# Performance work log

Measured on AMD Instinct MI355X. Metric: run time of the kernel, lower is better.

Reference implementation:

```python
import jax, jax.numpy as jnp
import numpy as np

STATE_DIM = 64
MEASURE_DIM = 32
N = 1048576  # measurement batch (broadcast column dim of z)


def setup_inputs() -> dict:
    key = jax.random.key(0)
    kz, kf = jax.random.split(key)
    z = jax.random.normal(kz, (MEASURE_DIM, N), dtype=jnp.float32)
    # Parameters initialized as in AKF.__init__ (identity matrices), with a
    # small perturbation on F so the dynamics are non-trivial but S stays
    # well-conditioned for the inverse.
    F = jnp.eye(STATE_DIM, dtype=jnp.float32) + 0.01 * jax.random.normal(kf, (STATE_DIM, STATE_DIM), dtype=jnp.float32)
    H = jnp.eye(MEASURE_DIM, STATE_DIM, dtype=jnp.float32)
    Q = jnp.eye(STATE_DIM, dtype=jnp.float32)
    R = jnp.eye(MEASURE_DIM, dtype=jnp.float32)
    P = jnp.eye(STATE_DIM, dtype=jnp.float32)
    x = jnp.zeros((STATE_DIM, 1), dtype=jnp.float32)
    return {"z": z, "F": F, "H": H, "Q": Q, "R": R, "P": P, "x": x}


def reference(z, F, H, Q, R, P, x):
    # One Kalman filter update step (predict + correct), batched over N
    # measurement columns in z. Returns the updated state estimate, matching
    # the torch module's `return self.x`.
    x_pred = F @ x                      # [s, 1]
    P_pred = F @ P @ F.T + Q            # [s, s]
    y = z - H @ x_pred                  # [m, N] (broadcast of [m,1])
    S = H @ P_pred @ H.T + R            # [m, m]
    K = P_pred @ H.T @ jnp.linalg.inv(S)  # [s, m]
    x_new = x_pred + K @ y              # [s, N]
    return x_new
```

## Files before the change

### kernel.cpp

```cpp
#include <hip/hip_runtime.h>

#define SD 64
#define MD 32

__global__ __launch_bounds__(256) void akf_prepare(
    const float* __restrict__ F, const float* __restrict__ H,
    const float* __restrict__ Q, const float* __restrict__ R,
    const float* __restrict__ P, const float* __restrict__ x,
    float* __restrict__ Kb)
{
    __shared__ float sT[SD * SD];
    __shared__ float sPp[SD * SD];
    __shared__ float sHP[MD * SD];
    __shared__ float sAug[MD][2 * MD];
    __shared__ float sK[SD * MD];
    __shared__ float sxp[SD];
    __shared__ float sHx[MD];
    __shared__ float sfac[MD];
    __shared__ float spiv;

    const int tid = threadIdx.x;

    if (tid < SD) {
        float a = 0.f;
        for (int k = 0; k < SD; ++k) a += F[tid * SD + k] * x[k];
        sxp[tid] = a;
    }
    for (int idx = tid; idx < SD * SD; idx += 256) {
        int i = idx >> 6, j = idx & 63;
        float a = 0.f;
        for (int k = 0; k < SD; ++k) a += F[i * SD + k] * P[k * SD + j];
        sT[idx] = a;
    }
    __syncthreads();

    for (int idx = tid; idx < SD * SD; idx += 256) {
        int i = idx >> 6, j = idx & 63;
        float a = Q[idx];
        for (int k = 0; k < SD; ++k) a += sT[i * SD + k] * F[j * SD + k];
        sPp[idx] = a;
    }
    __syncthreads();

    for (int idx = tid; idx < MD * SD; idx += 256) {
        int i = idx >> 6, j = idx & 63;
        float a = 0.f;
        for (int k = 0; k < SD; ++k) a += H[i * SD + k] * sPp[k * SD + j];
        sHP[idx] = a;
    }
    if (tid < MD) {
        float a = 0.f;
        for (int k = 0; k < SD; ++k) a += H[tid * SD + k] * sxp[k];
        sHx[tid] = a;
    }
    __syncthreads();

    for (int idx = tid; idx < MD * MD; idx += 256) {
        int i = idx >> 5, j = idx & 31;
        float a = R[idx];
        for (int k = 0; k < SD; ++k) a += sHP[i * SD + k] * H[j * SD + k];
        sAug[i][j] = a;
        sAug[i][MD + j] = (i == j) ? 1.f : 0.f;
    }
    __syncthreads();

    for (int kp = 0; kp < MD; ++kp) {
        if (tid == 0) spiv = 1.f / sAug[kp][kp];
        __syncthreads();
        if (tid < 2 * MD) sAug[kp][tid] *= spiv;
        __syncthreads();
        if (tid < MD) sfac[tid] = (tid == kp) ? 0.f : sAug[tid][kp];
        __syncthreads();
        for (int idx = tid; idx < MD * 2 * MD; idx += 256) {
            int i = idx >> 6, j = idx & 63;
            if (i != kp) sAug[i][j] -= sfac[i] * sAug[kp][j];
        }
        __syncthreads();
    }

    for (int idx = tid; idx < SD * MD; idx += 256) {
        int i = idx >> 5, j = idx & 31;
        float a = 0.f;
        for (int k = 0; k < SD; ++k) a += sPp[i * SD + k] * H[j * SD + k];
        sT[idx] = a;
    }
    __syncthreads();

    for (int idx = tid; idx < SD * MD; idx += 256) {
        int i = idx >> 5, j = idx & 31;
        float a = 0.f;
        for (int k = 0; k < MD; ++k) a += sT[i * MD + k] * sAug[k][MD + j];
        sK[idx] = a;
        Kb[idx] = a;
    }
    __syncthreads();

    if (tid < SD) {
        float a = sxp[tid];
        for (int j = 0; j < MD; ++j) a -= sK[tid * MD + j] * sHx[j];
        Kb[SD * MD + tid] = a;
    }
}

__global__ __launch_bounds__(256) void akf_apply(
    const float* __restrict__ z, const float* __restrict__ Kb,
    float* __restrict__ out, int N)
{
    __shared__ float sK[SD * MD];
    __shared__ float sb[SD];

    const int tid = threadIdx.x;
    for (int idx = tid; idx < SD * MD; idx += 256) sK[idx] = Kb[idx];
    if (tid < SD) sb[tid] = Kb[SD * MD + tid];
    __syncthreads();

    const int c = (blockIdx.x * 256 + tid) * 4;
    if (c >= N) return;

    float4 zv[MD];
#pragma unroll
    for (int j = 0; j < MD; ++j)
        zv[j] = *(const float4*)(z + (size_t)j * N + c);

#pragma unroll 2
    for (int i = 0; i < SD; ++i) {
        const float bi = sb[i];
        float4 acc = make_float4(bi, bi, bi, bi);
#pragma unroll
        for (int j = 0; j < MD; j += 4) {
            const float4 k4 = *(const float4*)(&sK[i * MD + j]);
            acc.x = fmaf(k4.x, zv[j].x, acc.x);
            acc.y = fmaf(k4.x, zv[j].y, acc.y);
            acc.z = fmaf(k4.x, zv[j].z, acc.z);
            acc.w = fmaf(k4.x, zv[j].w, acc.w);
            acc.x = fmaf(k4.y, zv[j + 1].x, acc.x);
            acc.y = fmaf(k4.y, zv[j + 1].y, acc.y);
            acc.z = fmaf(k4.y, zv[j + 1].z, acc.z);
            acc.w = fmaf(k4.y, zv[j + 1].w, acc.w);
            acc.x = fmaf(k4.z, zv[j + 2].x, acc.x);
            acc.y = fmaf(k4.z, zv[j + 2].y, acc.y);
            acc.z = fmaf(k4.z, zv[j + 2].z, acc.z);
            acc.w = fmaf(k4.z, zv[j + 2].w, acc.w);
            acc.x = fmaf(k4.w, zv[j + 3].x, acc.x);
            acc.y = fmaf(k4.w, zv[j + 3].y, acc.y);
            acc.z = fmaf(k4.w, zv[j + 3].z, acc.z);
            acc.w = fmaf(k4.w, zv[j + 3].w, acc.w);
        }
        *(float4*)(out + (size_t)i * N + c) = acc;
    }
}

extern "C" void kernel_launch(void* const* d_in, const int* in_sizes, int n_in,
                              void* d_out, int out_size, void* d_ws, size_t ws_size,
                              hipStream_t stream)
{
    const float* z = (const float*)d_in[0];
    const float* F = (const float*)d_in[1];
    const float* H = (const float*)d_in[2];
    const float* Q = (const float*)d_in[3];
    const float* R = (const float*)d_in[4];
    const float* P = (const float*)d_in[5];
    const float* x = (const float*)d_in[6];
    float* out = (float*)d_out;
    float* Kb = (float*)d_ws;

    const int N = in_sizes[0] / MD;

    akf_prepare<<<1, 256, 0, stream>>>(F, H, Q, R, P, x, Kb);

    const int cols_per_block = 256 * 4;
    const int nblocks = (N + cols_per_block - 1) / cols_per_block;
    akf_apply<<<nblocks, 256, 0, stream>>>(z, Kb, out, N);
}
```

Baseline: 469.4 us.

## Rewrite prepare kernel with 1024 threads and shuffle-based inverse; stream apply kernel

```diff
diff --git a/kernel.cpp b/kernel.cpp
--- a/kernel.cpp
+++ b/kernel.cpp
@@ -3,101 +3,154 @@
 #define SD 64
 #define MD 32
 
-__global__ __launch_bounds__(256) void akf_prepare(
+typedef float f32x4 __attribute__((ext_vector_type(4)));
+
+__global__ __launch_bounds__(1024) void akf_prepare(
     const float* __restrict__ F, const float* __restrict__ H,
     const float* __restrict__ Q, const float* __restrict__ R,
     const float* __restrict__ P, const float* __restrict__ x,
     float* __restrict__ Kb)
 {
-    __shared__ float sT[SD * SD];
-    __shared__ float sPp[SD * SD];
-    __shared__ float sHP[MD * SD];
-    __shared__ float sAug[MD][2 * MD];
-    __shared__ float sK[SD * MD];
-    __shared__ float sxp[SD];
-    __shared__ float sHx[MD];
-    __shared__ float sfac[MD];
-    __shared__ float spiv;
+    __shared__ __align__(16) float sF [SD * SD];
+    __shared__ __align__(16) float sFt[SD * 68];
+    __shared__ __align__(16) float sP [SD * SD];
+    __shared__ __align__(16) float sT [SD * 68];
+    __shared__ __align__(16) float sPp[SD * 68];
+    __shared__ __align__(16) float sH [MD * SD];
+    __shared__ __align__(16) float sHt[SD * 36];
+    __shared__ __align__(16) float sA [SD * 36];
+    __shared__ __align__(16) float sS [MD * 33];
+    __shared__ __align__(16) float sSi[MD * 36];
+    __shared__ __align__(16) float sK [SD * 36];
+    __shared__ float sx[SD], sxp[SD], sHx[MD];
 
     const int tid = threadIdx.x;
+
+    for (int idx = tid; idx < SD * SD; idx += 1024) {
+        float f = F[idx], p = P[idx];
+        int i = idx >> 6, j = idx & 63;
+        sF[idx] = f;
+        sFt[j * 68 + i] = f;
+        sP[idx] = p;
+    }
+    for (int idx = tid; idx < MD * SD; idx += 1024) {
+        float h = H[idx];
+        int j = idx >> 6, k = idx & 63;
+        sH[idx] = h;
+        sHt[k * 36 + j] = h;
+    }
+    if (tid < SD) sx[tid] = x[tid];
+    __syncthreads();
 
     if (tid < SD) {
         float a = 0.f;
-        for (int k = 0; k < SD; ++k) a += F[tid * SD + k] * x[k];
+        for (int k = 0; k < SD; ++k) a = fmaf(sFt[k * 68 + tid], sx[k], a);
         sxp[tid] = a;
     }
-    for (int idx = tid; idx < SD * SD; idx += 256) {
-        int i = idx >> 6, j = idx & 63;
-        float a = 0.f;
-        for (int k = 0; k < SD; ++k) a += F[i * SD + k] * P[k * SD + j];
-        sT[idx] = a;
-    }
-    __syncthreads();
-
-    for (int idx = tid; idx < SD * SD; idx += 256) {
-        int i = idx >> 6, j = idx & 63;
-        float a = Q[idx];
-        for (int k = 0; k < SD; ++k) a += sT[i * SD + k] * F[j * SD + k];
-        sPp[idx] = a;
-    }
-    __syncthreads();
-
-    for (int idx = tid; idx < MD * SD; idx += 256) {
-        int i = idx >> 6, j = idx & 63;
-        float a = 0.f;
-        for (int k = 0; k < SD; ++k) a += H[i * SD + k] * sPp[k * SD + j];
-        sHP[idx] = a;
-    }
+
+    {
+        const int i = tid >> 4, j0 = (tid & 15) * 4;
+        f32x4 acc = {0.f, 0.f, 0.f, 0.f};
+        for (int k = 0; k < SD; ++k) {
+            const float f = sF[i * 64 + k];
+            const f32x4 p4 = *(const f32x4*)&sP[k * 64 + j0];
+            acc.x = fmaf(f, p4.x, acc.x);
+            acc.y = fmaf(f, p4.y, acc.y);
+            acc.z = fmaf(f, p4.z, acc.z);
+            acc.w = fmaf(f, p4.w, acc.w);
+        }
+        *(f32x4*)&sT[i * 68 + j0] = acc;
+    }
+    __syncthreads();
+
+    {
+        const int i = tid >> 4, j0 = (tid & 15) * 4;
+        f32x4 acc = *(const f32x4*)&Q[i * 64 + j0];
+        for (int k = 0; k < SD; ++k) {
+            const float t = sT[i * 68 + k];
+            const f32x4 f4 = *(const f32x4*)&sFt[k * 68 + j0];
+            acc.x = fmaf(t, f4.x, acc.x);
+            acc.y = fmaf(t, f4.y, acc.y);
+            acc.z = fmaf(t, f4.z, acc.z);
+            acc.w = fmaf(t, f4.w, acc.w);
+        }
+        *(f32x4*)&sPp[i * 68 + j0] = acc;
+    }
+    __syncthreads();
+
     if (tid < MD) {
         float a = 0.f;
-        for (int k = 0; k < SD; ++k) a += H[tid * SD + k] * sxp[k];
+        for (int k = 0; k < SD; ++k) a = fmaf(sHt[k * 36 + tid], sxp[k], a);
         sHx[tid] = a;
     }
-    __syncthreads();
-
-    for (int idx = tid; idx < MD * MD; idx += 256) {
-        int i = idx >> 5, j = idx & 31;
-        float a = R[idx];
-        for (int k = 0; k < SD; ++k) a += sHP[i * SD + k] * H[j * SD + k];
-        sAug[i][j] = a;
-        sAug[i][MD + j] = (i == j) ? 1.f : 0.f;
-    }
-    __syncthreads();
-
-    for (int kp = 0; kp < MD; ++kp) {
-        if (tid == 0) spiv = 1.f / sAug[kp][kp];
-        __syncthreads();
-        if (tid < 2 * MD) sAug[kp][tid] *= spiv;
-        __syncthreads();
-        if (tid < MD) sfac[tid] = (tid == kp) ? 0.f : sAug[tid][kp];
-        __syncthreads();
-        for (int idx = tid; idx < MD * 2 * MD; idx += 256) {
-            int i = idx >> 6, j = idx & 63;
-            if (i != kp) sAug[i][j] -= sfac[i] * sAug[kp][j];
-        }
-        __syncthreads();
-    }
-
-    for (int idx = tid; idx < SD * MD; idx += 256) {
-        int i = idx >> 5, j = idx & 31;
-        float a = 0.f;
-        for (int k = 0; k < SD; ++k) a += sPp[i * SD + k] * H[j * SD + k];
-        sT[idx] = a;
-    }
-    __syncthreads();
-
-    for (int idx = tid; idx < SD * MD; idx += 256) {
-        int i = idx >> 5, j = idx & 31;
-        float a = 0.f;
-        for (int k = 0; k < MD; ++k) a += sT[i * MD + k] * sAug[k][MD + j];
-        sK[idx] = a;
-        Kb[idx] = a;
+    if (tid < 512) {
+        const int i = tid >> 3, j0 = (tid & 7) * 4;
+        f32x4 acc = {0.f, 0.f, 0.f, 0.f};
+        for (int k = 0; k < SD; ++k) {
+            const float p = sPp[i * 68 + k];
+            const f32x4 h4 = *(const f32x4*)&sHt[k * 36 + j0];
+            acc.x = fmaf(p, h4.x, acc.x);
+            acc.y = fmaf(p, h4.y, acc.y);
+            acc.z = fmaf(p, h4.z, acc.z);
+            acc.w = fmaf(p, h4.w, acc.w);
+        }
+        *(f32x4*)&sA[i * 36 + j0] = acc;
+    }
+    __syncthreads();
+
+    {
+        const int i = tid >> 5, j = tid & 31;
+        float a = R[i * 32 + j];
+        for (int k = 0; k < SD; ++k) a = fmaf(sH[i * 64 + k], sA[k * 36 + j], a);
+        sS[i * 33 + j] = a;
+    }
+    __syncthreads();
+
+    if (tid < 64) {
+        float col[MD];
+#pragma unroll
+        for (int i = 0; i < MD; ++i)
+            col[i] = (tid < MD) ? sS[i * 33 + tid] : ((i == tid - MD) ? 1.f : 0.f);
+#pragma unroll
+        for (int kp = 0; kp < MD; ++kp) {
+            const float piv = __shfl(col[kp], kp);
+            const float r = 1.0f / piv;
+            col[kp] *= r;
+            const float pr = col[kp];
+#pragma unroll
+            for (int i = 0; i < MD; ++i) {
+                if (i == kp) continue;
+                const float f = __shfl(col[i], kp);
+                col[i] = fmaf(-f, pr, col[i]);
+            }
+        }
+        if (tid >= MD) {
+            const int j = tid - MD;
+#pragma unroll
+            for (int i = 0; i < MD; ++i) sSi[i * 36 + j] = col[i];
+        }
+    }
+    __syncthreads();
+
+    if (tid < 512) {
+        const int i = tid >> 3, j0 = (tid & 7) * 4;
+        f32x4 acc = {0.f, 0.f, 0.f, 0.f};
+        for (int k = 0; k < MD; ++k) {
+            const float a = sA[i * 36 + k];
+            const f32x4 s4 = *(const f32x4*)&sSi[k * 36 + j0];
+            acc.x = fmaf(a, s4.x, acc.x);
+            acc.y = fmaf(a, s4.y, acc.y);
+            acc.z = fmaf(a, s4.z, acc.z);
+            acc.w = fmaf(a, s4.w, acc.w);
+        }
+        *(f32x4*)&sK[i * 36 + j0] = acc;
+        *(f32x4*)&Kb[i * MD + j0] = acc;
     }
     __syncthreads();
 
     if (tid < SD) {
         float a = sxp[tid];
-        for (int j = 0; j < MD; ++j) a -= sK[tid * MD + j] * sHx[j];
+        for (int j = 0; j < MD; ++j) a = fmaf(-sK[tid * 36 + j], sHx[j], a);
         Kb[SD * MD + tid] = a;
     }
 }
@@ -106,47 +159,32 @@
     const float* __restrict__ z, const float* __restrict__ Kb,
     float* __restrict__ out, int N)
 {
-    __shared__ float sK[SD * MD];
-    __shared__ float sb[SD];
-
-    const int tid = threadIdx.x;
-    for (int idx = tid; idx < SD * MD; idx += 256) sK[idx] = Kb[idx];
-    if (tid < SD) sb[tid] = Kb[SD * MD + tid];
-    __syncthreads();
-
-    const int c = (blockIdx.x * 256 + tid) * 4;
-    if (c >= N) return;
-
-    float4 zv[MD];
-#pragma unroll
-    for (int j = 0; j < MD; ++j)
-        zv[j] = *(const float4*)(z + (size_t)j * N + c);
-
-#pragma unroll 2
-    for (int i = 0; i < SD; ++i) {
-        const float bi = sb[i];
-        float4 acc = make_float4(bi, bi, bi, bi);
-#pragma unroll
-        for (int j = 0; j < MD; j += 4) {
-            const float4 k4 = *(const float4*)(&sK[i * MD + j]);
-            acc.x = fmaf(k4.x, zv[j].x, acc.x);
-            acc.y = fmaf(k4.x, zv[j].y, acc.y);
-            acc.z = fmaf(k4.x, zv[j].z, acc.z);
-            acc.w = fmaf(k4.x, zv[j].w, acc.w);
-            acc.x = fmaf(k4.y, zv[j + 1].x, acc.x);
-            acc.y = fmaf(k4.y, zv[j + 1].y, acc.y);
-            acc.z = fmaf(k4.y, zv[j + 1].z, acc.z);
-            acc.w = fmaf(k4.y, zv[j + 1].w, acc.w);
-            acc.x = fmaf(k4.z, zv[j + 2].x, acc.x);
-            acc.y = fmaf(k4.z, zv[j + 2].y, acc.y);
-            acc.z = fmaf(k4.z, zv[j + 2].z, acc.z);
-            acc.w = fmaf(k4.z, zv[j + 2].w, acc.w);
-            acc.x = fmaf(k4.w, zv[j + 3].x, acc.x);
-            acc.y = fmaf(k4.w, zv[j + 3].y, acc.y);
-            acc.z = fmaf(k4.w, zv[j + 3].z, acc.z);
-            acc.w = fmaf(k4.w, zv[j + 3].w, acc.w);
-        }
-        *(float4*)(out + (size_t)i * N + c) = acc;
+    const int base = blockIdx.x * (256 * 8) + threadIdx.x * 4;
+
+#pragma unroll 1
+    for (int g = 0; g < 2; ++g) {
+        const int c = base + g * (256 * 4);
+        if (c >= N) continue;
+
+        f32x4 zv[MD];
+#pragma unroll
+        for (int j = 0; j < MD; ++j)
+            zv[j] = __builtin_nontemporal_load((const f32x4*)(z + (size_t)j * N + c));
+
+#pragma unroll 4
+        for (int i = 0; i < SD; ++i) {
+            const float bi = Kb[SD * MD + i];
+            f32x4 acc = {bi, bi, bi, bi};
+#pragma unroll
+            for (int j = 0; j < MD; ++j) {
+                const float k = Kb[i * MD + j];
+                acc.x = fmaf(k, zv[j].x, acc.x);
+                acc.y = fmaf(k, zv[j].y, acc.y);
+                acc.z = fmaf(k, zv[j].z, acc.z);
+                acc.w = fmaf(k, zv[j].w, acc.w);
+            }
+            __builtin_nontemporal_store(acc, (f32x4*)(out + (size_t)i * N + c));
+        }
     }
 }
 
@@ -166,9 +204,9 @@
 
     const int N = in_sizes[0] / MD;
 
-    akf_prepare<<<1, 256, 0, stream>>>(F, H, Q, R, P, x, Kb);
-
-    const int cols_per_block = 256 * 4;
+    akf_prepare<<<1, 1024, 0, stream>>>(F, H, Q, R, P, x, Kb);
+
+    const int cols_per_block = 256 * 8;
     const int nblocks = (N + cols_per_block - 1) / cols_per_block;
     akf_apply<<<nblocks, 256, 0, stream>>>(z, Kb, out, N);
 }
```

New measurement: 399.5 us. 14.9% less time.
